# Optimization experiments

Measured on AMD Instinct MI355X. Metric: run time of the kernel, lower is better.

The kernel has to match this reference:

```python
import jax, jax.numpy as jnp
import numpy as np
import math

B, L, D_MODEL, D_HEAD = 4, 4096, 1024, 128

def setup_inputs() -> dict:
    key = jax.random.key(0)
    ks = jax.random.split(key, 9)
    s = 0.02
    return {
        "inp_q": jax.random.normal(ks[0], (B, L, D_MODEL), jnp.float32),
        "inp_k": jax.random.normal(ks[1], (B, L, D_MODEL), jnp.float32),
        "inp_v": jax.random.normal(ks[2], (B, L, D_MODEL), jnp.float32),
        "Wq": jax.random.normal(ks[3], (D_HEAD, D_MODEL), jnp.float32) * s,
        "bq": jax.random.normal(ks[4], (D_HEAD,), jnp.float32) * s,
        "Wk": jax.random.normal(ks[5], (D_HEAD, D_MODEL), jnp.float32) * s,
        "bk": jax.random.normal(ks[6], (D_HEAD,), jnp.float32) * s,
        "Wv": jax.random.normal(ks[7], (D_HEAD, D_MODEL), jnp.float32) * s,
        "bv": jax.random.normal(ks[8], (D_HEAD,), jnp.float32) * s,
    }

def reference(inp_q, inp_k, inp_v, Wq, bq, Wk, bk, Wv, bv):
    d_q = Wq.shape[0]
    # torch nn.Linear: y = x @ W.T + b
    Q = jnp.einsum('bld,qd->blq', inp_q, Wq) + bq   # [B, L, d_q]
    K = jnp.einsum('bld,kd->blk', inp_k, Wk) + bk   # [B, L, d_k]
    V = jnp.einsum('bld,vd->blv', inp_v, Wv) + bv   # [B, L, d_v]
    scores = jnp.einsum('bqe,bke->bqk', Q, K) / math.sqrt(d_q)  # [B, Lq, Lk]
    # NOTE: original uses nn.Softmax(dim=1) -> normalizes over the QUERY axis
    S = jax.nn.softmax(scores, axis=1)
    H = jnp.einsum('bqk,bkv->bqv', S, V)            # [B, Lq, d_v]
    return H
```

## Files before the change

kernel.cpp:

```cpp
#include <hip/hip_runtime.h>
#include <hip/hip_bf16.h>

#define B_  4
#define L_  4096
#define DM  1024
#define DH  128
#define KS  4
#define QS  4

#define SC2 0.12752844f

typedef __bf16 bf16_t;
typedef __attribute__((ext_vector_type(8))) __bf16 bf16x8;
typedef __attribute__((ext_vector_type(4))) __bf16 bf16x4;
typedef __attribute__((ext_vector_type(4))) float f32x4;

#if __has_builtin(__builtin_amdgcn_exp2f)
#define EXP2F(x) __builtin_amdgcn_exp2f(x)
#else
#define EXP2F(x) exp2f(x)
#endif

__device__ __forceinline__ f32x4 mfma16(bf16x8 a, bf16x8 b, f32x4 c) {
    return __builtin_amdgcn_mfma_f32_16x16x32_bf16(a, b, c, 0, 0, 0);
}

__device__ __forceinline__ int swz(int row, int rowbytes, int colbyte) {
    int slot = colbyte >> 4;
    return row * rowbytes + (((slot ^ (row & 7)) << 4) | (colbyte & 15));
}

__global__ __launch_bounds__(256) void proj_kernel(
    const float* __restrict__ Xq, const float* __restrict__ Xk, const float* __restrict__ Xv,
    const float* __restrict__ Wq, const float* __restrict__ Wk, const float* __restrict__ Wv,
    const float* __restrict__ bq, const float* __restrict__ bk, const float* __restrict__ bv,
    bf16_t* __restrict__ Q, bf16_t* __restrict__ K, bf16_t* __restrict__ V)
{
    const int which = blockIdx.y;
    const float* X    = which == 0 ? Xq : (which == 1 ? Xk : Xv);
    const float* W    = which == 0 ? Wq : (which == 1 ? Wk : Wv);
    const float* bias = which == 0 ? bq : (which == 1 ? bk : bv);
    bf16_t*      O    = which == 0 ? Q  : (which == 1 ? K  : V);

    __shared__ bf16_t Alds[64 * 64];
    __shared__ bf16_t Wlds[128 * 64];

    const int tid  = threadIdx.x;
    const int lane = tid & 63;
    const int wave = tid >> 6;
    const int wm = wave >> 1, wn = wave & 1;
    const int row0 = blockIdx.x * 64;

    f32x4 acc[2][4] = {};

    for (int kk = 0; kk < DM; kk += 64) {
        __syncthreads();
        #pragma unroll
        for (int it = 0; it < 4; ++it) {
            int id = it * 256 + tid;
            int r = id >> 4, c4 = id & 15;
            float4 v = *(const float4*)&X[(size_t)(row0 + r) * DM + kk + c4 * 4];
            bf16x4 bv4;
            bv4[0] = (__bf16)v.x; bv4[1] = (__bf16)v.y; bv4[2] = (__bf16)v.z; bv4[3] = (__bf16)v.w;
            *(bf16x4*)((char*)Alds + swz(r, 128, c4 * 8)) = bv4;
        }
        #pragma unroll
        for (int it = 0; it < 8; ++it) {
            int id = it * 256 + tid;
            int r = id >> 4, c4 = id & 15;
            float4 v = *(const float4*)&W[(size_t)r * DM + kk + c4 * 4];
            bf16x4 bv4;
            bv4[0] = (__bf16)v.x; bv4[1] = (__bf16)v.y; bv4[2] = (__bf16)v.z; bv4[3] = (__bf16)v.w;
            *(bf16x4*)((char*)Wlds + swz(r, 128, c4 * 8)) = bv4;
        }
        __syncthreads();
        #pragma unroll
        for (int ks = 0; ks < 2; ++ks) {
            bf16x8 af[2], bfr[4];
            #pragma unroll
            for (int mi = 0; mi < 2; ++mi) {
                int r = wm * 32 + mi * 16 + (lane & 15);
                af[mi] = *(const bf16x8*)((const char*)Alds + swz(r, 128, ks * 64 + (lane >> 4) * 16));
            }
            #pragma unroll
            for (int ni = 0; ni < 4; ++ni) {
                int r = wn * 64 + ni * 16 + (lane & 15);
                bfr[ni] = *(const bf16x8*)((const char*)Wlds + swz(r, 128, ks * 64 + (lane >> 4) * 16));
            }
            #pragma unroll
            for (int mi = 0; mi < 2; ++mi)
                #pragma unroll
                for (int ni = 0; ni < 4; ++ni)
                    acc[mi][ni] = mfma16(af[mi], bfr[ni], acc[mi][ni]);
        }
    }
    #pragma unroll
    for (int ni = 0; ni < 4; ++ni) {
        int h = wn * 64 + ni * 16 + (lane & 15);
        float bb = bias[h];
        #pragma unroll
        for (int mi = 0; mi < 2; ++mi)
            #pragma unroll
            for (int j = 0; j < 4; ++j) {
                int r = row0 + wm * 32 + mi * 16 + (lane >> 4) * 4 + j;
                O[(size_t)r * DH + h] = (__bf16)(acc[mi][ni][j] + bb);
            }
    }
}

__global__ __launch_bounds__(256) void stats_kernel(
    const bf16_t* __restrict__ Q, const bf16_t* __restrict__ K,
    float* __restrict__ Mpart, float* __restrict__ Lpart)
{
    const int b  = blockIdx.y;
    const int k0 = blockIdx.x * 64;
    const int qs = blockIdx.z;
    const int tid = threadIdx.x, lane = tid & 63, wave = tid >> 6;

    __shared__ bf16_t Klds[64 * 128];
    __shared__ bf16_t Qlds[128 * 128];

    const bf16_t* Kb = K + ((size_t)b * L_ + k0) * DH;
    #pragma unroll
    for (int it = 0; it < 4; ++it) {
        int id = it * 256 + tid;
        int r = id >> 4, s = id & 15;
        bf16x8 x = *(const bf16x8*)&Kb[(size_t)r * DH + s * 8];
        *(bf16x8*)((char*)Klds + swz(r, 256, s * 16)) = x;
    }
    __syncthreads();
    bf16x8 kfr[4][4];
    #pragma unroll
    for (int ni = 0; ni < 4; ++ni)
        #pragma unroll
        for (int ds = 0; ds < 4; ++ds) {
            int r = ni * 16 + (lane & 15);
            kfr[ni][ds] = *(const bf16x8*)((const char*)Klds + swz(r, 256, ds * 64 + (lane >> 4) * 16));
        }

    float mrun[4], lrun[4];
    #pragma unroll
    for (int ni = 0; ni < 4; ++ni) { mrun[ni] = -1e30f; lrun[ni] = 0.f; }

    const bf16_t* Qb = Q + (size_t)b * L_ * DH;
    const int qbase = qs * (L_ / QS);
    for (int q0 = qbase; q0 < qbase + L_ / QS; q0 += 128) {
        __syncthreads();
        #pragma unroll
        for (int it = 0; it < 8; ++it) {
            int id = it * 256 + tid;
            int r = id >> 4, s = id & 15;
            bf16x8 x = *(const bf16x8*)&Qb[(size_t)(q0 + r) * DH + s * 8];
            *(bf16x8*)((char*)Qlds + swz(r, 256, s * 16)) = x;
        }
        __syncthreads();
        f32x4 st[2][4] = {};
        #pragma unroll
        for (int mi = 0; mi < 2; ++mi)
            #pragma unroll
            for (int ds = 0; ds < 4; ++ds) {
                int r = wave * 32 + mi * 16 + (lane & 15);
                bf16x8 af = *(const bf16x8*)((const char*)Qlds + swz(r, 256, ds * 64 + (lane >> 4) * 16));
                #pragma unroll
                for (int ni = 0; ni < 4; ++ni)
                    st[mi][ni] = mfma16(af, kfr[ni][ds], st[mi][ni]);
            }
        #pragma unroll
        for (int ni = 0; ni < 4; ++ni) {
            float cm = -1e30f;
            #pragma unroll
            for (int mi = 0; mi < 2; ++mi)
                #pragma unroll
                for (int j = 0; j < 4; ++j) cm = fmaxf(cm, st[mi][ni][j]);
            cm *= SC2;
            cm = fmaxf(cm, __shfl_xor(cm, 16, 64));
            cm = fmaxf(cm, __shfl_xor(cm, 32, 64));
            float mnew = fmaxf(mrun[ni], cm);
            float p = 0.f;
            #pragma unroll
            for (int mi = 0; mi < 2; ++mi)
                #pragma unroll
                for (int j = 0; j < 4; ++j)
                    p += EXP2F(st[mi][ni][j] * SC2 - mnew);
            p += __shfl_xor(p, 16, 64);
            p += __shfl_xor(p, 32, 64);
            lrun[ni] = lrun[ni] * EXP2F(mrun[ni] - mnew) + p;
            mrun[ni] = mnew;
        }
    }
    __syncthreads();
    float* redm = (float*)Klds;
    float* redl = redm + 256;
    if (lane < 16) {
        #pragma unroll
        for (int ni = 0; ni < 4; ++ni) {
            redm[wave * 64 + ni * 16 + lane] = mrun[ni];
            redl[wave * 64 + ni * 16 + lane] = lrun[ni];
        }
    }
    __syncthreads();
    if (tid < 64) {
        float m0 = redm[tid], m1 = redm[64 + tid], m2v = redm[128 + tid], m3 = redm[192 + tid];
        float mt = fmaxf(fmaxf(m0, m1), fmaxf(m2v, m3));
        float lt = redl[tid]       * EXP2F(m0 - mt) + redl[64 + tid]  * EXP2F(m1 - mt)
                 + redl[128 + tid] * EXP2F(m2v - mt) + redl[192 + tid] * EXP2F(m3 - mt);
        Mpart[((size_t)qs * B_ + b) * L_ + k0 + tid] = mt;
        Lpart[((size_t)qs * B_ + b) * L_ + k0 + tid] = lt;
    }
}

__global__ __launch_bounds__(256) void comb_kernel(
    const float* __restrict__ Mpart, const float* __restrict__ Lpart,
    float* __restrict__ M2, float* __restrict__ Lsum)
{
    const size_t i = (size_t)blockIdx.x * 256 + threadIdx.x;
    const size_t N = (size_t)B_ * L_;
    float m = -1e30f;
    #pragma unroll
    for (int qs = 0; qs < QS; ++qs) m = fmaxf(m, Mpart[qs * N + i]);
    float l = 0.f;
    #pragma unroll
    for (int qs = 0; qs < QS; ++qs) l += Lpart[qs * N + i] * EXP2F(Mpart[qs * N + i] - m);
    M2[i] = m;
    Lsum[i] = l;
}

__global__ __launch_bounds__(256) void vt_kernel(
    const bf16_t* __restrict__ V, const float* __restrict__ Lsum, bf16_t* __restrict__ VT)
{
    const int b = blockIdx.z, v0 = blockIdx.y * 64, k0 = blockIdx.x * 64;
    __shared__ bf16_t tile[64][72];
    const int tid = threadIdx.x;
    const bf16_t* Vb = V + ((size_t)b * L_ + k0) * DH + v0;
    #pragma unroll
    for (int it = 0; it < 2; ++it) {
        int id = it * 256 + tid;
        int r = id >> 3, s = id & 7;
        bf16x8 x = *(const bf16x8*)&Vb[(size_t)r * DH + s * 8];
        *(bf16x8*)&tile[r][s * 8] = x;
    }
    __syncthreads();
    const int lane = tid & 63, wave = tid >> 6;
    float rl = 1.0f / Lsum[(size_t)b * L_ + k0 + lane];
    bf16_t* VTb = VT + ((size_t)b * DH + v0) * L_ + k0;
    #pragma unroll
    for (int i = 0; i < 16; ++i) {
        int v = wave * 16 + i;
        float x = (float)tile[lane][v];
        VTb[(size_t)v * L_ + lane] = (__bf16)(x * rl);
    }
}

__global__ __launch_bounds__(256) void pv_kernel(
    const bf16_t* __restrict__ Q, const bf16_t* __restrict__ K,
    const bf16_t* __restrict__ VT, const float* __restrict__ M2,
    float* __restrict__ out)
{
    const int b = blockIdx.y;
    const int q0 = blockIdx.x * 64;
    const int tid = threadIdx.x, lane = tid & 63, wave = tid >> 6;

    __shared__ bf16_t QPlds[64 * 128];
    __shared__ bf16_t Klds[64 * 128];
    __shared__ bf16_t VTlds[128 * 64];

    const bf16_t* Qb = Q + ((size_t)b * L_ + q0) * DH;
    #pragma unroll
    for (int it = 0; it < 4; ++it) {
        int id = it * 256 + tid;
        int r = id >> 4, s = id & 15;
        bf16x8 x = *(const bf16x8*)&Qb[(size_t)r * DH + s * 8];
        *(bf16x8*)((char*)QPlds + swz(r, 256, s * 16)) = x;
    }
    __syncthreads();
    bf16x8 qf[4][4];
    #pragma unroll
    for (int ni = 0; ni < 4; ++ni)
        #pragma unroll
        for (int ds = 0; ds < 4; ++ds) {
            int r = ni * 16 + (lane & 15);
            qf[ni][ds] = *(const bf16x8*)((const char*)QPlds + swz(r, 256, ds * 64 + (lane >> 4) * 16));
        }

    f32x4 acc[4][2] = {};
    const float*  m2b = M2 + (size_t)b * L_;
    const bf16_t* Kb  = K  + (size_t)b * L_ * DH;
    const bf16_t* VTb = VT + (size_t)b * DH * L_;
    bf16_t* Plds = QPlds;

    const int kbase = blockIdx.z * (L_ / KS);
    for (int kc = kbase; kc < kbase + L_ / KS; kc += 64) {
        __syncthreads();
        #pragma unroll
        for (int it = 0; it < 4; ++it) {
            int id = it * 256 + tid;
            int r = id >> 4, s = id & 15;
            bf16x8 x = *(const bf16x8*)&Kb[(size_t)(kc + r) * DH + s * 8];
            *(bf16x8*)((char*)Klds + swz(r, 256, s * 16)) = x;
        }
        #pragma unroll
        for (int it = 0; it < 4; ++it) {
            int id = it * 256 + tid;
            int r = id >> 3, s = id & 7;
            bf16x8 x = *(const bf16x8*)&VTb[(size_t)r * L_ + kc + s * 8];
            *(bf16x8*)((char*)VTlds + swz(r, 128, s * 16)) = x;
        }
        __syncthreads();
        f32x4 st[4] = {};
        #pragma unroll
        for (int ds = 0; ds < 4; ++ds) {
            int r = wave * 16 + (lane & 15);
            bf16x8 kf = *(const bf16x8*)((const char*)Klds + swz(r, 256, ds * 64 + (lane >> 4) * 16));
            #pragma unroll
            for (int ni = 0; ni < 4; ++ni)
                st[ni] = mfma16(kf, qf[ni][ds], st[ni]);
        }
        float4 mv = *(const float4*)&m2b[kc + wave * 16 + (lane >> 4) * 4];
        #pragma unroll
        for (int ni = 0; ni < 4; ++ni) {
            bf16x4 pk;
            pk[0] = (__bf16)EXP2F(st[ni][0] * SC2 - mv.x);
            pk[1] = (__bf16)EXP2F(st[ni][1] * SC2 - mv.y);
            pk[2] = (__bf16)EXP2F(st[ni][2] * SC2 - mv.z);
            pk[3] = (__bf16)EXP2F(st[ni][3] * SC2 - mv.w);
            int q = ni * 16 + (lane & 15);
            int colbyte = wave * 32 + (lane >> 4) * 8;
            *(bf16x4*)((char*)Plds + swz(q, 128, colbyte)) = pk;
        }
        __syncthreads();
        #pragma unroll
        for (int ks = 0; ks < 2; ++ks) {
            bf16x8 pf[4], vf[2];
            #pragma unroll
            for (int mi = 0; mi < 4; ++mi) {
                int q = mi * 16 + (lane & 15);
                pf[mi] = *(const bf16x8*)((const char*)Plds + swz(q, 128, ks * 64 + (lane >> 4) * 16));
            }
            #pragma unroll
            for (int ni = 0; ni < 2; ++ni) {
                int v = wave * 32 + ni * 16 + (lane & 15);
                vf[ni] = *(const bf16x8*)((const char*)VTlds + swz(v, 128, ks * 64 + (lane >> 4) * 16));
            }
            #pragma unroll
            for (int mi = 0; mi < 4; ++mi)
                #pragma unroll
                for (int ni = 0; ni < 2; ++ni)
                    acc[mi][ni] = mfma16(pf[mi], vf[ni], acc[mi][ni]);
        }
    }
    #pragma unroll
    for (int mi = 0; mi < 4; ++mi)
        #pragma unroll
        for (int ni = 0; ni < 2; ++ni)
            #pragma unroll
            for (int j = 0; j < 4; ++j) {
                int q = q0 + mi * 16 + (lane >> 4) * 4 + j;
                int v = wave * 32 + ni * 16 + (lane & 15);
                atomicAdd(&out[((size_t)b * L_ + q) * DH + v], acc[mi][ni][j]);
            }
}

extern "C" void kernel_launch(void* const* d_in, const int* in_sizes, int n_in,
                              void* d_out, int out_size, void* d_ws, size_t ws_size,
                              hipStream_t stream)
{
    const float* inq = (const float*)d_in[0];
    const float* ink = (const float*)d_in[1];
    const float* inv = (const float*)d_in[2];
    const float* Wq  = (const float*)d_in[3];
    const float* bq  = (const float*)d_in[4];
    const float* Wk  = (const float*)d_in[5];
    const float* bk  = (const float*)d_in[6];
    const float* Wv  = (const float*)d_in[7];
    const float* bv  = (const float*)d_in[8];
    float* out = (float*)d_out;

    const size_t nQKV = (size_t)B_ * L_ * DH;
    const size_t nBL  = (size_t)B_ * L_;
    char* ws = (char*)d_ws;
    bf16_t* Q  = (bf16_t*)ws;
    bf16_t* K  = Q + nQKV;
    bf16_t* V  = K + nQKV;
    bf16_t* VT = V + nQKV;
    float*  M2    = (float*)(VT + nQKV);
    float*  Lsum  = M2 + nBL;
    float*  Mpart = Lsum + nBL;
    float*  Lpart = Mpart + QS * nBL;

    hipMemsetAsync(out, 0, nQKV * sizeof(float), stream);
    proj_kernel<<<dim3(256, 3), 256, 0, stream>>>(inq, ink, inv, Wq, Wk, Wv, bq, bk, bv, Q, K, V);
    stats_kernel<<<dim3(L_ / 64, B_, QS), 256, 0, stream>>>(Q, K, Mpart, Lpart);
    comb_kernel<<<dim3(nBL / 256), 256, 0, stream>>>(Mpart, Lpart, M2, Lsum);
    vt_kernel<<<dim3(L_ / 64, DH / 64, B_), 256, 0, stream>>>(V, Lsum, VT);
    pv_kernel<<<dim3(L_ / 64, B_, KS), 256, 0, stream>>>(Q, K, VT, M2, out);
}
```

Baseline: 184.1 us.

## Pre-convert weights to bf16 and stage projection tiles via direct global-to-LDS loads

Adds a small kernel that converts the three fp32 weight matrices to bf16 once per call, stored in the VT workspace slot. The projection kernel then loads X (still fp32) and the bf16 weights straight into LDS with global_load_lds, using XOR-swizzled addressing, so tiles no longer pass through registers. X is converted to bf16 when fragments are read from LDS. This removes register staging and the repeated per-block weight conversion, at the cost of an extra launch, twice the LDS footprint for X, and conversion work inside the MFMA loop.

```diff
diff --git a/kernel.cpp b/kernel.cpp
--- a/kernel.cpp
+++ b/kernel.cpp
@@ -30,19 +30,40 @@
     return row * rowbytes + (((slot ^ (row & 7)) << 4) | (colbyte & 15));
 }
 
+__device__ __forceinline__ void gload_lds16(const void* g, void* l) {
+    __builtin_amdgcn_global_load_lds((const __attribute__((address_space(1))) void*)g,
+                                     (__attribute__((address_space(3))) void*)l, 16, 0, 0);
+}
+
+__global__ __launch_bounds__(256) void wcvt_kernel(
+    const float* __restrict__ Wq, const float* __restrict__ Wk, const float* __restrict__ Wv,
+    bf16_t* __restrict__ Wb)
+{
+    int idx = (blockIdx.x * 256 + threadIdx.x) * 8;
+    int which = idx >> 17;
+    int rem = idx & 131071;
+    const float* W = which == 0 ? Wq : (which == 1 ? Wk : Wv);
+    float4 a = *(const float4*)&W[rem];
+    float4 b = *(const float4*)&W[rem + 4];
+    bf16x8 o;
+    o[0] = (__bf16)a.x; o[1] = (__bf16)a.y; o[2] = (__bf16)a.z; o[3] = (__bf16)a.w;
+    o[4] = (__bf16)b.x; o[5] = (__bf16)b.y; o[6] = (__bf16)b.z; o[7] = (__bf16)b.w;
+    *(bf16x8*)&Wb[idx] = o;
+}
+
 __global__ __launch_bounds__(256) void proj_kernel(
     const float* __restrict__ Xq, const float* __restrict__ Xk, const float* __restrict__ Xv,
-    const float* __restrict__ Wq, const float* __restrict__ Wk, const float* __restrict__ Wv,
+    const bf16_t* __restrict__ Wb,
     const float* __restrict__ bq, const float* __restrict__ bk, const float* __restrict__ bv,
     bf16_t* __restrict__ Q, bf16_t* __restrict__ K, bf16_t* __restrict__ V)
 {
     const int which = blockIdx.y;
     const float* X    = which == 0 ? Xq : (which == 1 ? Xk : Xv);
-    const float* W    = which == 0 ? Wq : (which == 1 ? Wk : Wv);
     const float* bias = which == 0 ? bq : (which == 1 ? bk : bv);
     bf16_t*      O    = which == 0 ? Q  : (which == 1 ? K  : V);
-
-    __shared__ bf16_t Alds[64 * 64];
+    const bf16_t* Wm  = Wb + (size_t)which * DH * DM;
+
+    __shared__ float  Xlds[64 * 64];
     __shared__ bf16_t Wlds[128 * 64];
 
     const int tid  = threadIdx.x;
@@ -56,22 +77,20 @@
     for (int kk = 0; kk < DM; kk += 64) {
         __syncthreads();
         #pragma unroll
-        for (int it = 0; it < 4; ++it) {
-            int id = it * 256 + tid;
-            int r = id >> 4, c4 = id & 15;
-            float4 v = *(const float4*)&X[(size_t)(row0 + r) * DM + kk + c4 * 4];
-            bf16x4 bv4;
-            bv4[0] = (__bf16)v.x; bv4[1] = (__bf16)v.y; bv4[2] = (__bf16)v.z; bv4[3] = (__bf16)v.w;
-            *(bf16x4*)((char*)Alds + swz(r, 128, c4 * 8)) = bv4;
-        }
-        #pragma unroll
-        for (int it = 0; it < 8; ++it) {
-            int id = it * 256 + tid;
-            int r = id >> 4, c4 = id & 15;
-            float4 v = *(const float4*)&W[(size_t)r * DM + kk + c4 * 4];
-            bf16x4 bv4;
-            bv4[0] = (__bf16)v.x; bv4[1] = (__bf16)v.y; bv4[2] = (__bf16)v.z; bv4[3] = (__bf16)v.w;
-            *(bf16x4*)((char*)Wlds + swz(r, 128, c4 * 8)) = bv4;
+        for (int j = 0; j < 4; ++j) {
+            int c = wave * 4 + j;
+            int r = c * 4 + (lane >> 4);
+            int s = lane & 15;
+            gload_lds16(&X[(size_t)(row0 + r) * DM + kk + ((s ^ (r & 7)) << 2)],
+                        (char*)Xlds + c * 1024);
+        }
+        #pragma unroll
+        for (int j = 0; j < 4; ++j) {
+            int c = wave * 4 + j;
+            int r = c * 8 + (lane >> 3);
+            int s = lane & 7;
+            gload_lds16(&Wm[(size_t)r * DM + kk + ((s ^ (r & 7)) << 3)],
+                        (char*)Wlds + c * 1024);
         }
         __syncthreads();
         #pragma unroll
@@ -80,12 +99,20 @@
             #pragma unroll
             for (int mi = 0; mi < 2; ++mi) {
                 int r = wm * 32 + mi * 16 + (lane & 15);
-                af[mi] = *(const bf16x8*)((const char*)Alds + swz(r, 128, ks * 64 + (lane >> 4) * 16));
+                int rx = r & 7;
+                int s0 = ks * 8 + (lane >> 4) * 2;
+                float4 x0 = *(const float4*)&Xlds[r * 64 + ((s0 ^ rx) << 2)];
+                float4 x1 = *(const float4*)&Xlds[r * 64 + (((s0 + 1) ^ rx) << 2)];
+                bf16x8 a;
+                a[0] = (__bf16)x0.x; a[1] = (__bf16)x0.y; a[2] = (__bf16)x0.z; a[3] = (__bf16)x0.w;
+                a[4] = (__bf16)x1.x; a[5] = (__bf16)x1.y; a[6] = (__bf16)x1.z; a[7] = (__bf16)x1.w;
+                af[mi] = a;
             }
             #pragma unroll
             for (int ni = 0; ni < 4; ++ni) {
                 int r = wn * 64 + ni * 16 + (lane & 15);
-                bfr[ni] = *(const bf16x8*)((const char*)Wlds + swz(r, 128, ks * 64 + (lane >> 4) * 16));
+                int t = ks * 4 + (lane >> 4);
+                bfr[ni] = *(const bf16x8*)((const char*)Wlds + r * 128 + ((t ^ (r & 7)) << 4));
             }
             #pragma unroll
             for (int mi = 0; mi < 2; ++mi)
@@ -386,9 +413,11 @@
     float*  Lsum  = M2 + nBL;
     float*  Mpart = Lsum + nBL;
     float*  Lpart = Mpart + QS * nBL;
+    bf16_t* Wbuf = VT;
 
     hipMemsetAsync(out, 0, nQKV * sizeof(float), stream);
-    proj_kernel<<<dim3(256, 3), 256, 0, stream>>>(inq, ink, inv, Wq, Wk, Wv, bq, bk, bv, Q, K, V);
+    wcvt_kernel<<<dim3(192), 256, 0, stream>>>(Wq, Wk, Wv, Wbuf);
+    proj_kernel<<<dim3(256, 3), 256, 0, stream>>>(inq, ink, inv, Wbuf, bq, bk, bv, Q, K, V);
     stats_kernel<<<dim3(L_ / 64, B_, QS), 256, 0, stream>>>(Q, K, Mpart, Lpart);
     comb_kernel<<<dim3(nBL / 256), 256, 0, stream>>>(Mpart, Lpart, M2, Lsum);
     vt_kernel<<<dim3(L_ / 64, DH / 64, B_), 256, 0, stream>>>(V, Lsum, VT);
```

Result: no change. 180.9 us (-1.8%).

## Pre-convert weights to bf16 and rewrite projection as LDS-free register-pipelined GEMM

Applied to the files above, without the earlier changes.

Adds a small kernel that converts the three weight matrices to bf16 once, stored in the VT buffer before that buffer is written. The projection kernel is rewritten to load X and W fragments straight from global memory into registers with double buffering and nontemporal X loads. This removes the LDS staging, the barriers and the repeated per-block fp32 weight conversion. It also doubles the key/query split factors (KS, QS) for the stats and PV kernels, which raises parallelism but adds more partial results to combine.

```diff
diff --git a/kernel.cpp b/kernel.cpp
--- a/kernel.cpp
+++ b/kernel.cpp
@@ -5,8 +5,8 @@
 #define L_  4096
 #define DM  1024
 #define DH  128
-#define KS  4
-#define QS  4
+#define KS  8
+#define QS  8
 
 #define SC2 0.12752844f
 
@@ -30,81 +30,99 @@
     return row * rowbytes + (((slot ^ (row & 7)) << 4) | (colbyte & 15));
 }
 
-__global__ __launch_bounds__(256) void proj_kernel(
+__device__ __forceinline__ bf16x8 cvt8v(f32x4 a, f32x4 b) {
+    bf16x8 v;
+    v[0] = (__bf16)a.x; v[1] = (__bf16)a.y; v[2] = (__bf16)a.z; v[3] = (__bf16)a.w;
+    v[4] = (__bf16)b.x; v[5] = (__bf16)b.y; v[6] = (__bf16)b.z; v[7] = (__bf16)b.w;
+    return v;
+}
+
+__global__ __launch_bounds__(256) void wcvt_kernel(
+    const float* __restrict__ Wq, const float* __restrict__ Wk, const float* __restrict__ Wv,
+    bf16_t* __restrict__ Wb)
+{
+    int idx = (blockIdx.x * 256 + threadIdx.x) * 8;
+    int which = idx >> 17;
+    int rem = idx & 131071;
+    const float* W = which == 0 ? Wq : (which == 1 ? Wk : Wv);
+    f32x4 a = *(const f32x4*)&W[rem];
+    f32x4 b = *(const f32x4*)&W[rem + 4];
+    *(bf16x8*)&Wb[idx] = cvt8v(a, b);
+}
+
+__global__ __launch_bounds__(128) void projd_kernel(
     const float* __restrict__ Xq, const float* __restrict__ Xk, const float* __restrict__ Xv,
-    const float* __restrict__ Wq, const float* __restrict__ Wk, const float* __restrict__ Wv,
+    const bf16_t* __restrict__ Wb,
     const float* __restrict__ bq, const float* __restrict__ bk, const float* __restrict__ bv,
     bf16_t* __restrict__ Q, bf16_t* __restrict__ K, bf16_t* __restrict__ V)
 {
     const int which = blockIdx.y;
     const float* X    = which == 0 ? Xq : (which == 1 ? Xk : Xv);
-    const float* W    = which == 0 ? Wq : (which == 1 ? Wk : Wv);
     const float* bias = which == 0 ? bq : (which == 1 ? bk : bv);
     bf16_t*      O    = which == 0 ? Q  : (which == 1 ? K  : V);
-
-    __shared__ bf16_t Alds[64 * 64];
-    __shared__ bf16_t Wlds[128 * 64];
-
-    const int tid  = threadIdx.x;
-    const int lane = tid & 63;
-    const int wave = tid >> 6;
-    const int wm = wave >> 1, wn = wave & 1;
-    const int row0 = blockIdx.x * 64;
-
-    f32x4 acc[2][4] = {};
-
-    for (int kk = 0; kk < DM; kk += 64) {
-        __syncthreads();
-        #pragma unroll
-        for (int it = 0; it < 4; ++it) {
-            int id = it * 256 + tid;
-            int r = id >> 4, c4 = id & 15;
-            float4 v = *(const float4*)&X[(size_t)(row0 + r) * DM + kk + c4 * 4];
-            bf16x4 bv4;
-            bv4[0] = (__bf16)v.x; bv4[1] = (__bf16)v.y; bv4[2] = (__bf16)v.z; bv4[3] = (__bf16)v.w;
-            *(bf16x4*)((char*)Alds + swz(r, 128, c4 * 8)) = bv4;
-        }
-        #pragma unroll
-        for (int it = 0; it < 8; ++it) {
-            int id = it * 256 + tid;
-            int r = id >> 4, c4 = id & 15;
-            float4 v = *(const float4*)&W[(size_t)r * DM + kk + c4 * 4];
-            bf16x4 bv4;
-            bv4[0] = (__bf16)v.x; bv4[1] = (__bf16)v.y; bv4[2] = (__bf16)v.z; bv4[3] = (__bf16)v.w;
-            *(bf16x4*)((char*)Wlds + swz(r, 128, c4 * 8)) = bv4;
-        }
-        __syncthreads();
-        #pragma unroll
-        for (int ks = 0; ks < 2; ++ks) {
-            bf16x8 af[2], bfr[4];
-            #pragma unroll
-            for (int mi = 0; mi < 2; ++mi) {
-                int r = wm * 32 + mi * 16 + (lane & 15);
-                af[mi] = *(const bf16x8*)((const char*)Alds + swz(r, 128, ks * 64 + (lane >> 4) * 16));
-            }
-            #pragma unroll
-            for (int ni = 0; ni < 4; ++ni) {
-                int r = wn * 64 + ni * 16 + (lane & 15);
-                bfr[ni] = *(const bf16x8*)((const char*)Wlds + swz(r, 128, ks * 64 + (lane >> 4) * 16));
-            }
-            #pragma unroll
-            for (int mi = 0; mi < 2; ++mi)
-                #pragma unroll
-                for (int ni = 0; ni < 4; ++ni)
-                    acc[mi][ni] = mfma16(af[mi], bfr[ni], acc[mi][ni]);
-        }
-    }
-    #pragma unroll
-    for (int ni = 0; ni < 4; ++ni) {
-        int h = wn * 64 + ni * 16 + (lane & 15);
-        float bb = bias[h];
-        #pragma unroll
-        for (int mi = 0; mi < 2; ++mi)
-            #pragma unroll
-            for (int j = 0; j < 4; ++j) {
-                int r = row0 + wm * 32 + mi * 16 + (lane >> 4) * 4 + j;
-                O[(size_t)r * DH + h] = (__bf16)(acc[mi][ni][j] + bb);
-            }
+    const bf16_t* Wm  = Wb + (size_t)which * DH * DM;
+
+    const int lane = threadIdx.x & 63;
+    const int wave = threadIdx.x >> 6;
+    const int i16 = lane & 15, g4 = lane >> 4;
+    const int mbase = blockIdx.x * 32 + wave * 16;
+
+    const float*  xp = X  + (size_t)(mbase + i16) * DM + g4 * 8;
+    const bf16_t* wp = Wm + (size_t)i16 * DM + g4 * 8;
+
+    f32x4 acc[8] = {};
+
+    f32x4 xaA = __builtin_nontemporal_load((const f32x4*)xp);
+    f32x4 xbA = __builtin_nontemporal_load((const f32x4*)(xp + 4));
+    bf16x8 wA[8];
+    #pragma unroll
+    for (int ni = 0; ni < 8; ++ni)
+        wA[ni] = *(const bf16x8*)(wp + (size_t)ni * 16 * DM);
+
+    f32x4 xaB, xbB;
+    bf16x8 wB[8];
+
+    for (int s = 0; s < 32; s += 2) {
+        {
+            const float*  xn = xp + (s + 1) * 32;
+            const bf16_t* wn_ = wp + (s + 1) * 32;
+            xaB = __builtin_nontemporal_load((const f32x4*)xn);
+            xbB = __builtin_nontemporal_load((const f32x4*)(xn + 4));
+            #pragma unroll
+            for (int ni = 0; ni < 8; ++ni)
+                wB[ni] = *(const bf16x8*)(wn_ + (size_t)ni * 16 * DM);
+        }
+        {
+            bf16x8 af = cvt8v(xaA, xbA);
+            #pragma unroll
+            for (int ni = 0; ni < 8; ++ni)
+                acc[ni] = mfma16(af, wA[ni], acc[ni]);
+        }
+        if (s + 2 < 32) {
+            const float*  xn = xp + (s + 2) * 32;
+            const bf16_t* wn_ = wp + (s + 2) * 32;
+            xaA = __builtin_nontemporal_load((const f32x4*)xn);
+            xbA = __builtin_nontemporal_load((const f32x4*)(xn + 4));
+            #pragma unroll
+            for (int ni = 0; ni < 8; ++ni)
+                wA[ni] = *(const bf16x8*)(wn_ + (size_t)ni * 16 * DM);
+        }
+        {
+            bf16x8 af = cvt8v(xaB, xbB);
+            #pragma unroll
+            for (int ni = 0; ni < 8; ++ni)
+                acc[ni] = mfma16(af, wB[ni], acc[ni]);
+        }
+    }
+
+    #pragma unroll
+    for (int ni = 0; ni < 8; ++ni) {
+        float bb = bias[ni * 16 + i16];
+        #pragma unroll
+        for (int j = 0; j < 4; ++j) {
+            int r = mbase + g4 * 4 + j;
+            O[(size_t)r * DH + ni * 16 + i16] = (__bf16)(acc[ni][j] + bb);
+        }
     }
 }
 
@@ -315,7 +333,7 @@
             for (int ni = 0; ni < 4; ++ni)
                 st[ni] = mfma16(kf, qf[ni][ds], st[ni]);
         }
-        float4 mv = *(const float4*)&m2b[kc + wave * 16 + (lane >> 4) * 4];
+        f32x4 mv = *(const f32x4*)&m2b[kc + wave * 16 + (lane >> 4) * 4];
         #pragma unroll
         for (int ni = 0; ni < 4; ++ni) {
             bf16x4 pk;
@@ -386,9 +404,11 @@
     float*  Lsum  = M2 + nBL;
     float*  Mpart = Lsum + nBL;
     float*  Lpart = Mpart + QS * nBL;
-
-    hipMemsetAsync(out, 0, nQKV * sizeof(float), stream);
-    proj_kernel<<<dim3(256, 3), 256, 0, stream>>>(inq, ink, inv, Wq, Wk, Wv, bq, bk, bv, Q, K, V);
+    bf16_t* Wbuf = VT;
+
+    (void)hipMemsetAsync(out, 0, nQKV * sizeof(float), stream);
+    wcvt_kernel<<<dim3(192), 256, 0, stream>>>(Wq, Wk, Wv, Wbuf);
+    projd_kernel<<<dim3(512, 3), 128, 0, stream>>>(inq, ink, inv, Wbuf, bq, bk, bv, Q, K, V);
     stats_kernel<<<dim3(L_ / 64, B_, QS), 256, 0, stream>>>(Q, K, Mpart, Lpart);
     comb_kernel<<<dim3(nBL / 256), 256, 0, stream>>>(Mpart, Lpart, M2, Lsum);
     vt_kernel<<<dim3(L_ / 64, DH / 64, B_), 256, 0, stream>>>(V, Lsum, VT);
```

After: 263.4 us. 43.1% more time.
